# Performance work log

Measured on AMD Instinct MI355X. Metric: run time of the kernel, lower is better.

The kernel has to match this reference:

```python
import jax, jax.numpy as jnp
import numpy as np

DIM = 100
SAMPLE_DS = 0.5
MAX_S = int(DIM / SAMPLE_DS) + 1  # 201, matches torch sample_ds_arr
DIRECTIONS = ['x', 'x', 'y', 'y']  # constant in the original forward


def _polygon_area(poly):
    # poly: [bs, num_v, 2]; shoelace-style area identical to torch loop
    y_max = jnp.max(poly[:, :, 1], axis=-1)            # [bs]
    x0 = poly[:, :, 0]; y0 = poly[:, :, 1]
    x1 = jnp.roll(x0, -1, axis=1); y1 = jnp.roll(y0, -1, axis=1)
    s = jnp.sum((x1 - x0) * (y_max[:, None] - (y1 + y0) * 0.5), axis=1)
    return jnp.abs(s)


def _line_sum(mask_m, x0, x1, y0, y1, axis_x):
    # mask_m: [bs, DIM, DIM]; x0,x1,y0,y1: [bs, num_v]
    # Vectorized version of torch get_samples + interpolated_sum:
    # masked_select/dedup are replaced by boolean keep masks (samples along an
    # edge are monotone, so the valid set is a contiguous run and "previous
    # compacted sample" == "previous step").
    steps = jnp.arange(MAX_S, dtype=mask_m.dtype)      # [S]
    vx = x1 - x0 + 1e-6
    vy = y1 - y0 + 1e-6
    n = jnp.sqrt(vx * vx + vy * vy)
    vx = vx / n; vy = vy / n
    xs = x0[..., None] + steps * vx[..., None]         # [bs, nv, S]
    ys = y0[..., None] + steps * vy[..., None]
    xlo = jnp.minimum(x0, x1)[..., None]; xhi = jnp.maximum(x0, x1)[..., None]
    ylo = jnp.minimum(y0, y1)[..., None]; yhi = jnp.maximum(y0, y1)[..., None]
    seg = ((xs <= xhi + 1e-3) & (xs >= xlo - 1e-3) &
           (ys <= yhi + 1e-3) & (ys >= ylo - 1e-3))
    u = xs if axis_x else ys
    bound = (u <= DIM - 1) & (u >= 0.0)
    valid = seg & bound
    # dedup on floor(u) along sample axis (torch get_uniques)
    fu = jnp.floor(u)
    prev_valid = jnp.pad(valid[..., :-1], ((0, 0), (0, 0), (1, 0)))
    prev_fu = jnp.pad(fu[..., :-1], ((0, 0), (0, 0), (1, 0)))
    first = valid & ~prev_valid
    keep = valid & (first | (fu != prev_fu))
    # bilinear interpolation (torch interpolated_sum)
    X0f = jnp.floor(xs); Y0f = jnp.floor(ys)
    w00 = (X0f + 1 - xs) * (Y0f + 1 - ys)
    w01 = (X0f + 1 - xs) * (ys - Y0f)
    w10 = (xs - X0f) * (Y0f + 1 - ys)
    w11 = (xs - X0f) * (ys - Y0f)
    Xi0 = jnp.clip(X0f, 0, DIM - 1).astype(jnp.int32)
    Xi1 = jnp.clip(X0f + 1, 0, DIM - 1).astype(jnp.int32)
    Yi0 = jnp.clip(Y0f, 0, DIM - 1).astype(jnp.int32)
    Yi1 = jnp.clip(Y0f + 1, 0, DIM - 1).astype(jnp.int32)
    gather = jax.vmap(lambda m, yy, xx: m[yy, xx])      # over batch
    val = (w00 * gather(mask_m, Yi0, Xi0) + w01 * gather(mask_m, Yi1, Xi0) +
           w10 * gather(mask_m, Yi0, Xi1) + w11 * gather(mask_m, Yi1, Xi1))
    return jnp.sum(jnp.where(keep, val, 0.0), axis=-1)  # [bs, nv]


def _polygon_area_mask(poly, gt_mask):
    # poly: [bs, nv, 2], gt_mask: [bs, 4, DIM, DIM]
    x0 = poly[:, :, 0]; y0 = poly[:, :, 1]
    x1 = jnp.roll(x0, -1, axis=1); y1 = jnp.roll(y0, -1, axis=1)
    ret = jnp.zeros(poly.shape[0], dtype=poly.dtype)
    for m, d in enumerate(DIRECTIONS):
        ax = (d == 'x')
        sign = jnp.where((x1 > x0) if ax else (y1 > y0), 1.0, -1.0)
        sf = _line_sum(gt_mask[:, m], x0, x1, y0, y1, ax)
        sb = _line_sum(gt_mask[:, m], x1, x0, y1, y0, ax)
        s = jnp.sum(sign * (sf + sb) * 0.5, axis=1)
        ret = ret + jnp.abs(s)
    return ret / len(DIRECTIONS)


def setup_inputs() -> dict:
    key = jax.random.key(0)
    k1, k2, k3 = jax.random.split(key, 3)
    bs, nv = 512, 64
    poly = jax.random.uniform(k1, (bs, nv, 2), dtype=jnp.float32) * (DIM - 1)
    gt = jax.random.uniform(k2, (bs, nv, 2), dtype=jnp.float32) * (DIM - 1)
    gt_mask = jax.random.uniform(k3, (bs, 4, DIM, DIM), dtype=jnp.float32)
    return {"poly": poly, "gt": gt, "gt_mask": gt_mask}


def reference(poly, gt, gt_mask):
    pred_area = _polygon_area(poly)
    gt_area = _polygon_area(gt)
    int_area = _polygon_area_mask(poly, gt_mask)
    union_area = pred_area + gt_area - int_area
    return int_area / union_area
```

## Files before the change

### kernel.cpp

```cpp
#include <hip/hip_runtime.h>
#include <math.h>

#define DIM   100
#define NV    64
#define BS    512
#define MAXCH 1664
#define SMW   108
#define SMH   103

template<bool AX>
__device__ __forceinline__ float mainloop(
    const unsigned char* sm, const float4* prmA, const float4* prmB,
    const unsigned short* chunkTab, int totE, int tid) {
  const int grp = tid >> 5;
  const int sub = (tid >> 3) & 3;
  const int st  = tid & 7;
  const int base0 = grp * 16 + sub * 4;
  float acc = 0.0f;

  for (int i = 0; i * 128 < totE; ++i) {
    const ushort4 ent = *reinterpret_cast<const ushort4*>(
        &chunkTab[i * 128 + base0]);

    #define SAMPLE(e) {                                                    \
      const int c = (e) >> 4;                                              \
      const float kf = (float)((((e) & 15) << 3) | st);                    \
      const float4 p = prmA[c];                                            \
      const float4 q = prmB[c];                                            \
      const float vu = AX ? p.z : p.w;                                     \
      const float u0 = AX ? p.x : p.y;                                     \
      const float fu0 = floorf(u0);                                        \
      const float ck = fu0 + __builtin_copysignf(kf, vu);                  \
      const float te = ceilf(fmaf(kf, q.z, q.w));                          \
      const float u1 = __fadd_rn(__fmul_rn(te, vu), u0);                   \
      float t = (floorf(u1) == ck) ? te : (te + 1.0f);                     \
      t = fmaxf(t, 0.0f);                                                  \
      const float xs = __fadd_rn(__fmul_rn(t, p.z), p.x);                  \
      const float ys = __fadd_rn(__fmul_rn(t, p.w), p.y);                  \
      const float X0 = floorf(xs), Y0 = floorf(ys);                        \
      const float wx1 = xs - X0, wy1 = ys - Y0;                            \
      const float wx0 = 1.0f - wx1, wy0 = 1.0f - wy1;                      \
      const int ix = max(min((int)X0, 100), -1);                           \
      const int iy = max(min((int)Y0, 100), -1);                           \
      const int a = iy * SMW + ix;                                         \
      const float g00 = (float)sm[a + (SMW + 4)];                          \
      const float g10 = (float)sm[a + (SMW + 5)];                          \
      const float g01 = (float)sm[a + (2 * SMW + 4)];                      \
      const float g11 = (float)sm[a + (2 * SMW + 5)];                      \
      const float top = fmaf(wx1, g10, wx0 * g00);                         \
      const float bot = fmaf(wx1, g11, wx0 * g01);                         \
      const float val = fmaf(wy1, bot, wy0 * top);                         \
      const float w = (kf <= q.y) ? q.x : 0.0f;                            \
      acc = fmaf(w, val, acc);                                             \
    }
    SAMPLE(ent.x); SAMPLE(ent.y); SAMPLE(ent.z); SAMPLE(ent.w);
    #undef SAMPLE
  }
  return acc;
}

__global__ __launch_bounds__(256, 8) void diffiou_intersect(
    const float* __restrict__ poly, const float* __restrict__ gt_mask,
    float* __restrict__ ws) {
  __shared__ unsigned char sm[SMH * SMW];
  __shared__ float4 prmA[128];
  __shared__ float4 prmB[128];
  __shared__ unsigned short chunkTab[MAXCH];
  __shared__ int   wsum[2];
  __shared__ int   totalChunks;
  __shared__ float red[4];

  const int bid = blockIdx.x;
  const int b   = bid >> 2;
  const int m   = bid & 3;
  const bool ax = (m < 2);
  const int tid = threadIdx.x;

  {
    const float* src = gt_mask + (size_t)(b * 4 + m) * (DIM * DIM);
    for (int j = tid; j < SMH * 25; j += 256) {
      const int r = j / 25;
      const int g = j - r * 25;
      const int sr = min(max(r - 1, 0), DIM - 1);
      const float4 v = *reinterpret_cast<const float4*>(&src[sr * DIM + 4 * g]);
      const unsigned int c0 = (unsigned int)__float2int_rn(v.x * 255.0f);
      const unsigned int c1 = (unsigned int)__float2int_rn(v.y * 255.0f);
      const unsigned int c2 = (unsigned int)__float2int_rn(v.z * 255.0f);
      const unsigned int c3 = (unsigned int)__float2int_rn(v.w * 255.0f);
      *reinterpret_cast<unsigned int*>(&sm[r * SMW + 4 + 4 * g]) =
          c0 | (c1 << 8) | (c2 << 16) | (c3 << 24);
    }
    for (int r = tid; r < SMH; r += 256) {
      const int sr = min(max(r - 1, 0), DIM - 1);
      const unsigned char e0 =
          (unsigned char)__float2int_rn(src[sr * DIM + 0] * 255.0f);
      const unsigned char e9 =
          (unsigned char)__float2int_rn(src[sr * DIM + DIM - 1] * 255.0f);
      sm[r * SMW + 3] = e0;
      sm[r * SMW + 104] = e9;
      sm[r * SMW + 105] = e9;
    }
    for (int j = tid; j < MAXCH; j += 256) chunkTab[j] = 15;
  }

  int ncv = 0;
  if (tid < 128) {
    const int e  = tid >> 1;
    const int fb = tid & 1;
    const float* pb = poly + (size_t)b * NV * 2;
    const float ex0 = pb[e * 2 + 0], ey0 = pb[e * 2 + 1];
    const int   en  = (e + 1) & (NV - 1);
    const float ex1 = pb[en * 2 + 0], ey1 = pb[en * 2 + 1];
    const float sign = (ax ? (ex1 > ex0) : (ey1 > ey0)) ? 1.0f : -1.0f;
    const float x0 = fb ? ex1 : ex0, y0 = fb ? ey1 : ey0;
    const float x1 = fb ? ex0 : ex1, y1 = fb ? ey0 : ey1;
    float vx = (x1 - x0) + 1e-6f;
    float vy = (y1 - y0) + 1e-6f;
    const float n = __fsqrt_rn(__fadd_rn(__fmul_rn(vx, vx), __fmul_rn(vy, vy)));
    vx = __fdiv_rn(vx, n);
    vy = __fdiv_rn(vy, n);
    float xlo = fminf(x0, x1) - 0.001f, xhi = fmaxf(x0, x1) + 0.001f;
    float ylo = fminf(y0, y1) - 0.001f, yhi = fmaxf(y0, y1) + 0.001f;
    if (ax) { xlo = fmaxf(xlo, 0.0f); xhi = fminf(xhi, (float)(DIM - 1)); }
    else    { ylo = fmaxf(ylo, 0.0f); yhi = fminf(yhi, (float)(DIM - 1)); }

    #define VALID_AT(tt, out) {                                   \
      const float tf_ = (float)(tt);                              \
      const float xs_ = __fadd_rn(__fmul_rn(tf_, vx), x0);        \
      const float ys_ = __fadd_rn(__fmul_rn(tf_, vy), y0);        \
      out = (xs_ <= xhi) && (xs_ >= xlo) &&                       \
            (ys_ <= yhi) && (ys_ >= ylo);                         \
    }
    int T;
    bool v200; VALID_AT(200, v200);
    if (v200) { T = 200; }
    else {
      int lo = 0, hi = 200;
      #pragma unroll
      for (int it = 0; it < 8; ++it) {
        const int mid = (lo + hi) >> 1;
        bool vm; VALID_AT(mid, vm);
        if (vm) lo = mid; else hi = mid;
      }
      T = lo;
    }
    #undef VALID_AT

    const float vu  = ax ? vx : vy;
    const float u0  = ax ? x0 : y0;
    const float fu0 = floorf(u0);
    const float uT  = __fadd_rn(__fmul_rn((float)T, vu), u0);
    int K = abs((int)floorf(uT) - (int)fu0);
    K = min(K, 99);
    const float B = __fdiv_rn(1.0f, fabsf(vu));
    const float D = (vu > 0.0f) ? (fu0 - u0) : (u0 - fu0 - 1.0f);
    prmA[tid] = make_float4(x0, y0, vx, vy);
    prmB[tid] = make_float4(sign * (0.5f / 255.0f), (float)K,
                            B, fmaf(D, B, -0.005f));
    ncv = (K >> 3) + 1;
  }

  int v = ncv;
  #pragma unroll
  for (int i = 1; i < 64; i <<= 1) {
    const int w = __shfl_up(v, i, 64);
    if ((tid & 63) >= i) v += w;
  }
  if (((tid & 63) == 63) && (tid < 128)) wsum[tid >> 6] = v;
  __syncthreads();
  if ((tid >= 64) && (tid < 128)) v += wsum[0];
  if (tid < 128) {
    const int start = v - ncv;
    for (int k = 0; k < ncv; ++k)
      chunkTab[start + k] = (unsigned short)((tid << 4) | k);
    if (tid == 127) totalChunks = v;
  }
  __syncthreads();

  const int totE = totalChunks;
  const float acc = ax ? mainloop<true >(sm, prmA, prmB, chunkTab, totE, tid)
                       : mainloop<false>(sm, prmA, prmB, chunkTab, totE, tid);

  float a = acc;
  #pragma unroll
  for (int o = 32; o > 0; o >>= 1) a += __shfl_xor(a, o, 64);
  if ((tid & 63) == 0) red[tid >> 6] = a;
  __syncthreads();
  if (tid == 0) {
    const float s = red[0] + red[1] + red[2] + red[3];
    ws[bid] = fabsf(s);
  }
}

__device__ __forceinline__ float wave_area(const float* P, int b, int v) {
  const float x0 = P[(size_t)(b * NV + v) * 2 + 0];
  const float y0 = P[(size_t)(b * NV + v) * 2 + 1];
  const int vn = (v + 1) & (NV - 1);
  const float x1 = P[(size_t)(b * NV + vn) * 2 + 0];
  const float y1 = P[(size_t)(b * NV + vn) * 2 + 1];
  float ym = y0;
  #pragma unroll
  for (int o = 32; o > 0; o >>= 1) ym = fmaxf(ym, __shfl_xor(ym, o, 64));
  float term = (x1 - x0) * (ym - (y1 + y0) * 0.5f);
  #pragma unroll
  for (int o = 32; o > 0; o >>= 1) term += __shfl_xor(term, o, 64);
  return fabsf(term);
}

__global__ __launch_bounds__(64) void diffiou_finalize(
    const float* __restrict__ poly, const float* __restrict__ gt,
    const float* __restrict__ ws, float* __restrict__ out) {
  const int b = blockIdx.x;
  const int v = threadIdx.x;
  const float pa = wave_area(poly, b, v);
  const float ga = wave_area(gt, b, v);
  if (v == 0) {
    const float ia = 0.25f * (ws[b * 4 + 0] + ws[b * 4 + 1] +
                              ws[b * 4 + 2] + ws[b * 4 + 3]);
    out[b] = ia / (pa + ga - ia);
  }
}

extern "C" void kernel_launch(void* const* d_in, const int* in_sizes, int n_in,
                              void* d_out, int out_size, void* d_ws, size_t ws_size,
                              hipStream_t stream) {
  const float* poly    = (const float*)d_in[0];
  const float* gt      = (const float*)d_in[1];
  const float* gt_mask = (const float*)d_in[2];
  float* out = (float*)d_out;
  float* ws  = (float*)d_ws;

  hipLaunchKernelGGL(diffiou_intersect, dim3(BS * 4), dim3(256), 0, stream,
                     poly, gt_mask, ws);
  hipLaunchKernelGGL(diffiou_finalize, dim3(BS), dim3(64), 0, stream,
                     poly, gt, ws, out);
}
```

Before: 33.65 us.

## Fuse finalize into intersect kernel via last-block atomic counter; shrink per-edge params

Replaces the separate finalize launch with a last-arriving-block pattern: each of the four per-batch blocks publishes its partial sum and bumps an atomic counter, and the fourth computes the polygon areas and IoU output. A memset of the counters is added in place of the second kernel launch. Separately, the per-edge prmB float4 is reduced to a single packed float (sign and K), and B and D are recomputed in the inner loop with a fast reciprocal. This trades LDS traffic for extra ALU work per sample and may change rounding.

```diff
diff --git a/kernel.cpp b/kernel.cpp
--- a/kernel.cpp
+++ b/kernel.cpp
@@ -7,10 +7,11 @@
 #define MAXCH 1664
 #define SMW   108
 #define SMH   103
+#define SHWC  (0.5f / 255.0f)
 
 template<bool AX>
 __device__ __forceinline__ float mainloop(
-    const unsigned char* sm, const float4* prmA, const float4* prmB,
+    const unsigned char* sm, const float4* prmA, const float* meta,
     const unsigned short* chunkTab, int totE, int tid) {
   const int grp = tid >> 5;
   const int sub = (tid >> 3) & 3;
@@ -25,13 +26,15 @@
     #define SAMPLE(e) {                                                    \
       const int c = (e) >> 4;                                              \
       const float kf = (float)((((e) & 15) << 3) | st);                    \
-      const float4 p = prmA[c];                                            \
-      const float4 q = prmB[c];                                            \
+      const float4 p = prmA[c];                          \
+      const float mt = meta[c];                          \
       const float vu = AX ? p.z : p.w;                                     \
       const float u0 = AX ? p.x : p.y;                                     \
       const float fu0 = floorf(u0);                                        \
+      const float Bv = __builtin_amdgcn_rcpf(fabsf(vu));                   \
+      const float D  = (vu > 0.0f) ? (fu0 - u0) : (u0 - fu0 - 1.0f);       \
+      const float te = ceilf((kf + D) * Bv - 0.005f);                      \
       const float ck = fu0 + __builtin_copysignf(kf, vu);                  \
-      const float te = ceilf(fmaf(kf, q.z, q.w));                          \
       const float u1 = __fadd_rn(__fmul_rn(te, vu), u0);                   \
       float t = (floorf(u1) == ck) ? te : (te + 1.0f);                     \
       t = fmaxf(t, 0.0f);                                                  \
@@ -50,7 +53,8 @@
       const float top = fmaf(wx1, g10, wx0 * g00);                         \
       const float bot = fmaf(wx1, g11, wx0 * g01);                         \
       const float val = fmaf(wy1, bot, wy0 * top);                         \
-      const float w = (kf <= q.y) ? q.x : 0.0f;                            \
+      const float w = (kf < fabsf(mt)) ? __builtin_copysignf(SHWC, mt)     \
+                                       : 0.0f;                             \
       acc = fmaf(w, val, acc);                                             \
     }
     SAMPLE(ent.x); SAMPLE(ent.y); SAMPLE(ent.z); SAMPLE(ent.w);
@@ -59,16 +63,34 @@
   return acc;
 }
 
+__device__ __forceinline__ float wave_area(const float* P, int b, int v) {
+  const float x0 = P[(size_t)(b * NV + v) * 2 + 0];
+  const float y0 = P[(size_t)(b * NV + v) * 2 + 1];
+  const int vn = (v + 1) & (NV - 1);
+  const float x1 = P[(size_t)(b * NV + vn) * 2 + 0];
+  const float y1 = P[(size_t)(b * NV + vn) * 2 + 1];
+  float ym = y0;
+  #pragma unroll
+  for (int o = 32; o > 0; o >>= 1) ym = fmaxf(ym, __shfl_xor(ym, o, 64));
+  float term = (x1 - x0) * (ym - (y1 + y0) * 0.5f);
+  #pragma unroll
+  for (int o = 32; o > 0; o >>= 1) term += __shfl_xor(term, o, 64);
+  return fabsf(term);
+}
+
+template<bool FUSED>
 __global__ __launch_bounds__(256, 8) void diffiou_intersect(
-    const float* __restrict__ poly, const float* __restrict__ gt_mask,
-    float* __restrict__ ws) {
+    const float* __restrict__ poly, const float* __restrict__ gt,
+    const float* __restrict__ gt_mask,
+    float* __restrict__ ws, int* __restrict__ cnt, float* __restrict__ out) {
   __shared__ unsigned char sm[SMH * SMW];
   __shared__ float4 prmA[128];
-  __shared__ float4 prmB[128];
+  __shared__ float  meta[128];
   __shared__ unsigned short chunkTab[MAXCH];
   __shared__ int   wsum[2];
   __shared__ int   totalChunks;
   __shared__ float red[4];
+  __shared__ int   flag;
 
   const int bid = blockIdx.x;
   const int b   = bid >> 2;
@@ -124,12 +146,12 @@
     if (ax) { xlo = fmaxf(xlo, 0.0f); xhi = fminf(xhi, (float)(DIM - 1)); }
     else    { ylo = fmaxf(ylo, 0.0f); yhi = fminf(yhi, (float)(DIM - 1)); }
 
-    #define VALID_AT(tt, out) {                                   \
+    #define VALID_AT(tt, out_) {                                  \
       const float tf_ = (float)(tt);                              \
       const float xs_ = __fadd_rn(__fmul_rn(tf_, vx), x0);        \
       const float ys_ = __fadd_rn(__fmul_rn(tf_, vy), y0);        \
-      out = (xs_ <= xhi) && (xs_ >= xlo) &&                       \
-            (ys_ <= yhi) && (ys_ >= ylo);                         \
+      out_ = (xs_ <= xhi) && (xs_ >= xlo) &&                      \
+             (ys_ <= yhi) && (ys_ >= ylo);                        \
     }
     int T;
     bool v200; VALID_AT(200, v200);
@@ -152,11 +174,8 @@
     const float uT  = __fadd_rn(__fmul_rn((float)T, vu), u0);
     int K = abs((int)floorf(uT) - (int)fu0);
     K = min(K, 99);
-    const float B = __fdiv_rn(1.0f, fabsf(vu));
-    const float D = (vu > 0.0f) ? (fu0 - u0) : (u0 - fu0 - 1.0f);
     prmA[tid] = make_float4(x0, y0, vx, vy);
-    prmB[tid] = make_float4(sign * (0.5f / 255.0f), (float)K,
-                            B, fmaf(D, B, -0.005f));
+    meta[tid] = sign * ((float)K + 0.5f);
     ncv = (K >> 3) + 1;
   }
 
@@ -178,33 +197,45 @@
   __syncthreads();
 
   const int totE = totalChunks;
-  const float acc = ax ? mainloop<true >(sm, prmA, prmB, chunkTab, totE, tid)
-                       : mainloop<false>(sm, prmA, prmB, chunkTab, totE, tid);
+  const float acc = ax ? mainloop<true >(sm, prmA, meta, chunkTab, totE, tid)
+                       : mainloop<false>(sm, prmA, meta, chunkTab, totE, tid);
 
   float a = acc;
   #pragma unroll
   for (int o = 32; o > 0; o >>= 1) a += __shfl_xor(a, o, 64);
   if ((tid & 63) == 0) red[tid >> 6] = a;
   __syncthreads();
+
+  if (!FUSED) {
+    if (tid == 0) ws[bid] = fabsf(red[0] + red[1] + red[2] + red[3]);
+    return;
+  }
+
   if (tid == 0) {
-    const float s = red[0] + red[1] + red[2] + red[3];
-    ws[bid] = fabsf(s);
-  }
-}
-
-__device__ __forceinline__ float wave_area(const float* P, int b, int v) {
-  const float x0 = P[(size_t)(b * NV + v) * 2 + 0];
-  const float y0 = P[(size_t)(b * NV + v) * 2 + 1];
-  const int vn = (v + 1) & (NV - 1);
-  const float x1 = P[(size_t)(b * NV + vn) * 2 + 0];
-  const float y1 = P[(size_t)(b * NV + vn) * 2 + 1];
-  float ym = y0;
-  #pragma unroll
-  for (int o = 32; o > 0; o >>= 1) ym = fmaxf(ym, __shfl_xor(ym, o, 64));
-  float term = (x1 - x0) * (ym - (y1 + y0) * 0.5f);
-  #pragma unroll
-  for (int o = 32; o > 0; o >>= 1) term += __shfl_xor(term, o, 64);
-  return fabsf(term);
+    const float s = fabsf(red[0] + red[1] + red[2] + red[3]);
+    __hip_atomic_store(&ws[bid], s, __ATOMIC_RELEASE,
+                       __HIP_MEMORY_SCOPE_AGENT);
+    const int old = __hip_atomic_fetch_add(&cnt[b], 1, __ATOMIC_ACQ_REL,
+                                           __HIP_MEMORY_SCOPE_AGENT);
+    flag = (old == 3);
+  }
+  __syncthreads();
+  if (flag && tid < 64) {
+    const float pa = wave_area(poly, b, tid);
+    const float ga = wave_area(gt,   b, tid);
+    if (tid == 0) {
+      const float i0 = __hip_atomic_load(&ws[b * 4 + 0], __ATOMIC_ACQUIRE,
+                                         __HIP_MEMORY_SCOPE_AGENT);
+      const float i1 = __hip_atomic_load(&ws[b * 4 + 1], __ATOMIC_ACQUIRE,
+                                         __HIP_MEMORY_SCOPE_AGENT);
+      const float i2 = __hip_atomic_load(&ws[b * 4 + 2], __ATOMIC_ACQUIRE,
+                                         __HIP_MEMORY_SCOPE_AGENT);
+      const float i3 = __hip_atomic_load(&ws[b * 4 + 3], __ATOMIC_ACQUIRE,
+                                         __HIP_MEMORY_SCOPE_AGENT);
+      const float ia = 0.25f * (i0 + i1 + i2 + i3);
+      out[b] = ia / (pa + ga - ia);
+    }
+  }
 }
 
 __global__ __launch_bounds__(64) void diffiou_finalize(
@@ -229,9 +260,16 @@
   const float* gt_mask = (const float*)d_in[2];
   float* out = (float*)d_out;
   float* ws  = (float*)d_ws;
-
-  hipLaunchKernelGGL(diffiou_intersect, dim3(BS * 4), dim3(256), 0, stream,
-                     poly, gt_mask, ws);
-  hipLaunchKernelGGL(diffiou_finalize, dim3(BS), dim3(64), 0, stream,
-                     poly, gt, ws, out);
-}
+  int*   cnt = (int*)((char*)d_ws + 2048 * 4);
+
+  if (ws_size >= 2048 * 4 + 512 * 4) {
+    hipMemsetAsync(cnt, 0, 512 * sizeof(int), stream);
+    hipLaunchKernelGGL((diffiou_intersect<true>), dim3(BS * 4), dim3(256), 0,
+                       stream, poly, gt, gt_mask, ws, cnt, out);
+  } else {
+    hipLaunchKernelGGL((diffiou_intersect<false>), dim3(BS * 4), dim3(256), 0,
+                       stream, poly, gt, gt_mask, ws, cnt, out);
+    hipLaunchKernelGGL(diffiou_finalize, dim3(BS), dim3(64), 0, stream,
+                       poly, gt, ws, out);
+  }
+}
```

New measurement: 100.3 us. +198.1%, slower.

## Process both same-direction masks per block to share sample and weight computation

Applied to the files above, without the earlier changes.

Each block now handles two masks that share the same direction (x or y). It loads both into shared memory, computes the sample positions and bilinear weights once, and gathers from both masks. This halves the grid and removes duplicated setup work: the edge parameters, the binary search and the chunk table. In exchange it doubles shared memory per block, lowers the launch-bounds occupancy hint from 8 to 4, and gives the grid less parallelism.

```diff
diff --git a/kernel.cpp b/kernel.cpp
--- a/kernel.cpp
+++ b/kernel.cpp
@@ -7,16 +7,18 @@
 #define MAXCH 1664
 #define SMW   108
 #define SMH   103
+#define MSZ   (SMH * SMW)
 
 template<bool AX>
-__device__ __forceinline__ float mainloop(
+__device__ __forceinline__ void mainloop(
     const unsigned char* sm, const float4* prmA, const float4* prmB,
-    const unsigned short* chunkTab, int totE, int tid) {
+    const unsigned short* chunkTab, int totE, int tid,
+    float& acc0o, float& acc1o) {
   const int grp = tid >> 5;
   const int sub = (tid >> 3) & 3;
   const int st  = tid & 7;
   const int base0 = grp * 16 + sub * 4;
-  float acc = 0.0f;
+  float acc0 = 0.0f, acc1 = 0.0f;
 
   for (int i = 0; i * 128 < totE; ++i) {
     const ushort4 ent = *reinterpret_cast<const ushort4*>(
@@ -43,51 +45,61 @@
       const int ix = max(min((int)X0, 100), -1);                           \
       const int iy = max(min((int)Y0, 100), -1);                           \
       const int a = iy * SMW + ix;                                         \
-      const float g00 = (float)sm[a + (SMW + 4)];                          \
-      const float g10 = (float)sm[a + (SMW + 5)];                          \
-      const float g01 = (float)sm[a + (2 * SMW + 4)];                      \
-      const float g11 = (float)sm[a + (2 * SMW + 5)];                      \
-      const float top = fmaf(wx1, g10, wx0 * g00);                         \
-      const float bot = fmaf(wx1, g11, wx0 * g01);                         \
-      const float val = fmaf(wy1, bot, wy0 * top);                         \
+      const float g00a = (float)sm[a + (SMW + 4)];                         \
+      const float g10a = (float)sm[a + (SMW + 5)];                         \
+      const float g01a = (float)sm[a + (2 * SMW + 4)];                     \
+      const float g11a = (float)sm[a + (2 * SMW + 5)];                     \
+      const float g00b = (float)sm[a + (MSZ + SMW + 4)];                   \
+      const float g10b = (float)sm[a + (MSZ + SMW + 5)];                   \
+      const float g01b = (float)sm[a + (MSZ + 2 * SMW + 4)];               \
+      const float g11b = (float)sm[a + (MSZ + 2 * SMW + 5)];               \
+      const float topa = fmaf(wx1, g10a, wx0 * g00a);                      \
+      const float bota = fmaf(wx1, g11a, wx0 * g01a);                      \
+      const float vala = fmaf(wy1, bota, wy0 * topa);                      \
+      const float topb = fmaf(wx1, g10b, wx0 * g00b);                      \
+      const float botb = fmaf(wx1, g11b, wx0 * g01b);                      \
+      const float valb = fmaf(wy1, botb, wy0 * topb);                      \
       const float w = (kf <= q.y) ? q.x : 0.0f;                            \
-      acc = fmaf(w, val, acc);                                             \
+      acc0 = fmaf(w, vala, acc0);                                          \
+      acc1 = fmaf(w, valb, acc1);                                          \
     }
     SAMPLE(ent.x); SAMPLE(ent.y); SAMPLE(ent.z); SAMPLE(ent.w);
     #undef SAMPLE
   }
-  return acc;
-}
-
-__global__ __launch_bounds__(256, 8) void diffiou_intersect(
+  acc0o = acc0; acc1o = acc1;
+}
+
+__global__ __launch_bounds__(256, 4) void diffiou_intersect(
     const float* __restrict__ poly, const float* __restrict__ gt_mask,
     float* __restrict__ ws) {
-  __shared__ unsigned char sm[SMH * SMW];
+  __shared__ unsigned char sm[2 * MSZ];
   __shared__ float4 prmA[128];
   __shared__ float4 prmB[128];
   __shared__ unsigned short chunkTab[MAXCH];
   __shared__ int   wsum[2];
   __shared__ int   totalChunks;
-  __shared__ float red[4];
-
-  const int bid = blockIdx.x;
-  const int b   = bid >> 2;
-  const int m   = bid & 3;
-  const bool ax = (m < 2);
+  __shared__ float red[4][2];
+
+  const int g   = blockIdx.x;
+  const int b   = g >> 1;
+  const int mb  = (g & 1) * 2;
+  const bool ax = (mb == 0);
   const int tid = threadIdx.x;
 
-  {
-    const float* src = gt_mask + (size_t)(b * 4 + m) * (DIM * DIM);
+  #pragma unroll
+  for (int s = 0; s < 2; ++s) {
+    const float* src = gt_mask + (size_t)(b * 4 + mb + s) * (DIM * DIM);
+    unsigned char* dst = sm + s * MSZ;
     for (int j = tid; j < SMH * 25; j += 256) {
       const int r = j / 25;
-      const int g = j - r * 25;
+      const int q = j - r * 25;
       const int sr = min(max(r - 1, 0), DIM - 1);
-      const float4 v = *reinterpret_cast<const float4*>(&src[sr * DIM + 4 * g]);
+      const float4 v = *reinterpret_cast<const float4*>(&src[sr * DIM + 4 * q]);
       const unsigned int c0 = (unsigned int)__float2int_rn(v.x * 255.0f);
       const unsigned int c1 = (unsigned int)__float2int_rn(v.y * 255.0f);
       const unsigned int c2 = (unsigned int)__float2int_rn(v.z * 255.0f);
       const unsigned int c3 = (unsigned int)__float2int_rn(v.w * 255.0f);
-      *reinterpret_cast<unsigned int*>(&sm[r * SMW + 4 + 4 * g]) =
+      *reinterpret_cast<unsigned int*>(&dst[r * SMW + 4 + 4 * q]) =
           c0 | (c1 << 8) | (c2 << 16) | (c3 << 24);
     }
     for (int r = tid; r < SMH; r += 256) {
@@ -96,12 +108,12 @@
           (unsigned char)__float2int_rn(src[sr * DIM + 0] * 255.0f);
       const unsigned char e9 =
           (unsigned char)__float2int_rn(src[sr * DIM + DIM - 1] * 255.0f);
-      sm[r * SMW + 3] = e0;
-      sm[r * SMW + 104] = e9;
-      sm[r * SMW + 105] = e9;
-    }
-    for (int j = tid; j < MAXCH; j += 256) chunkTab[j] = 15;
-  }
+      dst[r * SMW + 3] = e0;
+      dst[r * SMW + 104] = e9;
+      dst[r * SMW + 105] = e9;
+    }
+  }
+  for (int j = tid; j < MAXCH; j += 256) chunkTab[j] = 15;
 
   int ncv = 0;
   if (tid < 128) {
@@ -124,12 +136,12 @@
     if (ax) { xlo = fmaxf(xlo, 0.0f); xhi = fminf(xhi, (float)(DIM - 1)); }
     else    { ylo = fmaxf(ylo, 0.0f); yhi = fminf(yhi, (float)(DIM - 1)); }
 
-    #define VALID_AT(tt, out) {                                   \
+    #define VALID_AT(tt, out_) {                                  \
       const float tf_ = (float)(tt);                              \
       const float xs_ = __fadd_rn(__fmul_rn(tf_, vx), x0);        \
       const float ys_ = __fadd_rn(__fmul_rn(tf_, vy), y0);        \
-      out = (xs_ <= xhi) && (xs_ >= xlo) &&                       \
-            (ys_ <= yhi) && (ys_ >= ylo);                         \
+      out_ = (xs_ <= xhi) && (xs_ >= xlo) &&                      \
+             (ys_ <= yhi) && (ys_ >= ylo);                        \
     }
     int T;
     bool v200; VALID_AT(200, v200);
@@ -178,17 +190,22 @@
   __syncthreads();
 
   const int totE = totalChunks;
-  const float acc = ax ? mainloop<true >(sm, prmA, prmB, chunkTab, totE, tid)
-                       : mainloop<false>(sm, prmA, prmB, chunkTab, totE, tid);
-
-  float a = acc;
-  #pragma unroll
-  for (int o = 32; o > 0; o >>= 1) a += __shfl_xor(a, o, 64);
-  if ((tid & 63) == 0) red[tid >> 6] = a;
+  float acc0, acc1;
+  if (ax) mainloop<true >(sm, prmA, prmB, chunkTab, totE, tid, acc0, acc1);
+  else    mainloop<false>(sm, prmA, prmB, chunkTab, totE, tid, acc0, acc1);
+
+  #pragma unroll
+  for (int o = 32; o > 0; o >>= 1) {
+    acc0 += __shfl_xor(acc0, o, 64);
+    acc1 += __shfl_xor(acc1, o, 64);
+  }
+  if ((tid & 63) == 0) { red[tid >> 6][0] = acc0; red[tid >> 6][1] = acc1; }
   __syncthreads();
   if (tid == 0) {
-    const float s = red[0] + red[1] + red[2] + red[3];
-    ws[bid] = fabsf(s);
+    const float s0 = red[0][0] + red[1][0] + red[2][0] + red[3][0];
+    const float s1 = red[0][1] + red[1][1] + red[2][1] + red[3][1];
+    ws[b * 4 + mb + 0] = fabsf(s0);
+    ws[b * 4 + mb + 1] = fabsf(s1);
   }
 }
 
@@ -230,7 +247,7 @@
   float* out = (float*)d_out;
   float* ws  = (float*)d_ws;
 
-  hipLaunchKernelGGL(diffiou_intersect, dim3(BS * 4), dim3(256), 0, stream,
+  hipLaunchKernelGGL(diffiou_intersect, dim3(BS * 2), dim3(256), 0, stream,
                      poly, gt_mask, ws);
   hipLaunchKernelGGL(diffiou_finalize, dim3(BS), dim3(64), 0, stream,
                      poly, gt, ws, out);
```

Result: slower. 43.46 us (+29.2%).

## Prefetch mask tiles into registers and overlap conversion with edge setup

Applied to the files above, without the earlier changes.

The grid-strided loop that loaded the 100x100 mask tile into shared memory is replaced by explicit register prefetches of float4 words, issued in two batches. The first batch's loads are in flight while the per-edge parameter setup and binary search run, and the second batch is fetched before the prefix scan, so global-memory latency is hidden behind that compute. The full chunk-table initialization is replaced by padding only the tail up to the next multiple of 128, which needs an extra barrier. Register pressure rises because of the ten live float4 values, and that could hurt occupancy under the 256x8 launch bounds.

```diff
diff --git a/kernel.cpp b/kernel.cpp
--- a/kernel.cpp
+++ b/kernel.cpp
@@ -76,31 +76,24 @@
   const bool ax = (m < 2);
   const int tid = threadIdx.x;
 
-  {
-    const float* src = gt_mask + (size_t)(b * 4 + m) * (DIM * DIM);
-    for (int j = tid; j < SMH * 25; j += 256) {
-      const int r = j / 25;
-      const int g = j - r * 25;
-      const int sr = min(max(r - 1, 0), DIM - 1);
-      const float4 v = *reinterpret_cast<const float4*>(&src[sr * DIM + 4 * g]);
-      const unsigned int c0 = (unsigned int)__float2int_rn(v.x * 255.0f);
-      const unsigned int c1 = (unsigned int)__float2int_rn(v.y * 255.0f);
-      const unsigned int c2 = (unsigned int)__float2int_rn(v.z * 255.0f);
-      const unsigned int c3 = (unsigned int)__float2int_rn(v.w * 255.0f);
-      *reinterpret_cast<unsigned int*>(&sm[r * SMW + 4 + 4 * g]) =
-          c0 | (c1 << 8) | (c2 << 16) | (c3 << 24);
-    }
-    for (int r = tid; r < SMH; r += 256) {
-      const int sr = min(max(r - 1, 0), DIM - 1);
-      const unsigned char e0 =
-          (unsigned char)__float2int_rn(src[sr * DIM + 0] * 255.0f);
-      const unsigned char e9 =
-          (unsigned char)__float2int_rn(src[sr * DIM + DIM - 1] * 255.0f);
-      sm[r * SMW + 3] = e0;
-      sm[r * SMW + 104] = e9;
-      sm[r * SMW + 105] = e9;
-    }
-    for (int j = tid; j < MAXCH; j += 256) chunkTab[j] = 15;
+  const float*  src  = gt_mask + (size_t)(b * 4 + m) * (DIM * DIM);
+  const float4* src4 = reinterpret_cast<const float4*>(src);
+
+  float4 L0 = src4[tid];
+  float4 L1 = src4[tid + 256];
+  float4 L2 = src4[tid + 512];
+  float4 L3 = src4[tid + 768];
+  float4 L4 = src4[tid + 1024];
+
+  #define CVTW(L, j) {                                                     \
+    const int r_ = (j) / 25;                                               \
+    const int g_ = (j) - r_ * 25;                                          \
+    const unsigned int c0 = (unsigned int)__float2int_rn((L).x * 255.0f);  \
+    const unsigned int c1 = (unsigned int)__float2int_rn((L).y * 255.0f);  \
+    const unsigned int c2 = (unsigned int)__float2int_rn((L).z * 255.0f);  \
+    const unsigned int c3 = (unsigned int)__float2int_rn((L).w * 255.0f);  \
+    *reinterpret_cast<unsigned int*>(&sm[(r_ + 1) * SMW + 4 + 4 * g_]) =   \
+        c0 | (c1 << 8) | (c2 << 16) | (c3 << 24);                          \
   }
 
   int ncv = 0;
@@ -124,12 +117,12 @@
     if (ax) { xlo = fmaxf(xlo, 0.0f); xhi = fminf(xhi, (float)(DIM - 1)); }
     else    { ylo = fmaxf(ylo, 0.0f); yhi = fminf(yhi, (float)(DIM - 1)); }
 
-    #define VALID_AT(tt, out) {                                   \
+    #define VALID_AT(tt, out_) {                                  \
       const float tf_ = (float)(tt);                              \
       const float xs_ = __fadd_rn(__fmul_rn(tf_, vx), x0);        \
       const float ys_ = __fadd_rn(__fmul_rn(tf_, vy), y0);        \
-      out = (xs_ <= xhi) && (xs_ >= xlo) &&                       \
-            (ys_ <= yhi) && (ys_ >= ylo);                         \
+      out_ = (xs_ <= xhi) && (xs_ >= xlo) &&                      \
+             (ys_ <= yhi) && (ys_ >= ylo);                        \
     }
     int T;
     bool v200; VALID_AT(200, v200);
@@ -160,6 +153,19 @@
     ncv = (K >> 3) + 1;
   }
 
+  CVTW(L0, tid);
+  CVTW(L1, tid + 256);
+  CVTW(L2, tid + 512);
+  CVTW(L3, tid + 768);
+  CVTW(L4, tid + 1024);
+  const int j5 = tid + 1280, j6 = tid + 1536, j7 = tid + 1792,
+            j8 = tid + 2048, j9 = tid + 2304;
+  L0 = src4[j5];
+  L1 = src4[j6];
+  L2 = src4[j7];
+  L3 = src4[j8];
+  L4 = (j9 < 2500) ? src4[j9] : make_float4(0.f, 0.f, 0.f, 0.f);
+
   int v = ncv;
   #pragma unroll
   for (int i = 1; i < 64; i <<= 1) {
@@ -175,9 +181,43 @@
       chunkTab[start + k] = (unsigned short)((tid << 4) | k);
     if (tid == 127) totalChunks = v;
   }
+
+  CVTW(L0, j5);
+  CVTW(L1, j6);
+  CVTW(L2, j7);
+  CVTW(L3, j8);
+  if (j9 < 2500) CVTW(L4, j9);
+  if (tid < 75) {
+    const int rr = tid / 25;
+    const int g  = tid - rr * 25;
+    const int srow = (rr == 0) ? 0 : (DIM - 1);
+    const int drow = (rr == 0) ? 0 : (100 + rr);
+    const float4 q = src4[srow * 25 + g];
+    const unsigned int c0 = (unsigned int)__float2int_rn(q.x * 255.0f);
+    const unsigned int c1 = (unsigned int)__float2int_rn(q.y * 255.0f);
+    const unsigned int c2 = (unsigned int)__float2int_rn(q.z * 255.0f);
+    const unsigned int c3 = (unsigned int)__float2int_rn(q.w * 255.0f);
+    *reinterpret_cast<unsigned int*>(&sm[drow * SMW + 4 + 4 * g]) =
+        c0 | (c1 << 8) | (c2 << 16) | (c3 << 24);
+  }
+  if (tid < SMH) {
+    const int sr = min(max(tid - 1, 0), DIM - 1);
+    const unsigned char e0 =
+        (unsigned char)__float2int_rn(src[sr * DIM + 0] * 255.0f);
+    const unsigned char e9 =
+        (unsigned char)__float2int_rn(src[sr * DIM + DIM - 1] * 255.0f);
+    sm[tid * SMW + 3] = e0;
+    sm[tid * SMW + 104] = e9;
+    sm[tid * SMW + 105] = e9;
+  }
+  #undef CVTW
   __syncthreads();
 
   const int totE = totalChunks;
+  const int endE = (totE + 127) & ~127;
+  if (totE + tid < endE) chunkTab[totE + tid] = 15;
+  __syncthreads();
+
   const float acc = ax ? mainloop<true >(sm, prmA, prmB, chunkTab, totE, tid)
                        : mainloop<false>(sm, prmA, prmB, chunkTab, totE, tid);
 
```

Result: faster. 32.63 us (-3.0%).
